# Kernel tuning notes

Measured on AMD Instinct MI355X. Metric: run time of the kernel, lower is better.

Reference implementation:

```python
import jax, jax.numpy as jnp
import numpy as np

B, C1, C2 = 8, 256, 256
Cc = 128          # c = int(c2 * e)
RED = 16          # reduction in FrequencyModulation
HEADS = 8
HD = Cc // HEADS  # 16
HH, WW = 32, 32


def _c1x1(x, w, b=None):
    # 1x1 conv as channel contraction; w: [out_c, in_c]
    y = jnp.einsum('bchw,oc->bohw', x, w)
    return y if b is None else y + b[None, :, None, None]


def setup_inputs() -> dict:
    key = jax.random.key(0)
    ks = jax.random.split(key, 22)
    s = 0.02
    p = {}
    p['x'] = jax.random.normal(ks[0], (B, C1, HH, WW), jnp.float32)
    p['cv1_w'] = jax.random.normal(ks[1], (2 * Cc, C1), jnp.float32) * s
    p['cv1_b'] = jnp.zeros((2 * Cc,), jnp.float32)
    # FrequencyModulation params
    p['fm_w1'] = jax.random.normal(ks[2], (Cc // RED, Cc), jnp.float32) * s
    p['fm_w2'] = jax.random.normal(ks[3], (Cc, Cc // RED), jnp.float32) * s
    p['ca_w1'] = jax.random.normal(ks[4], (Cc // RED, Cc), jnp.float32) * s
    p['ca_w2'] = jax.random.normal(ks[5], (Cc, Cc // RED), jnp.float32) * s
    # TokenStatisticsSelfAttention params (qkv_bias=False)
    p['qkv_w'] = jax.random.normal(ks[6], (3 * Cc, Cc), jnp.float32) * s
    p['tproj_w'] = jax.random.normal(ks[7], (Cc, Cc), jnp.float32) * s
    p['tproj_b'] = jnp.zeros((Cc,), jnp.float32)
    # SpatialQuantizedRouter params
    p['dw_w'] = jax.random.normal(ks[8], (Cc, 1, 3, 3), jnp.float32) * s  # depthwise
    p['dw_b'] = jnp.zeros((Cc,), jnp.float32)
    p['rt_w'] = jax.random.normal(ks[9], (1, Cc), jnp.float32) * s
    p['rt_b'] = jnp.zeros((1,), jnp.float32)
    p['q_w'] = jax.random.normal(ks[10], (Cc, Cc), jnp.float32) * s
    p['k_w'] = jax.random.normal(ks[11], (Cc, Cc), jnp.float32) * s
    p['v_w'] = jax.random.normal(ks[12], (Cc, Cc), jnp.float32) * s
    p['sproj_w'] = jax.random.normal(ks[13], (Cc, Cc), jnp.float32) * s
    p['sproj_b'] = jnp.zeros((Cc,), jnp.float32)
    p['cv2_w'] = jax.random.normal(ks[14], (C2, 3 * Cc), jnp.float32) * s
    p['cv2_b'] = jnp.zeros((C2,), jnp.float32)
    return p


def _forward(x, cv1_w, cv1_b, fm_w1, fm_w2, ca_w1, ca_w2, qkv_w, tproj_w,
             tproj_b, dw_w, dw_b, rt_w, rt_b, q_w, k_w, v_w, sproj_w,
             sproj_b, cv2_w, cv2_b):
    Bb, _, H, W = x.shape
    N = H * W
    y = _c1x1(x, cv1_w, cv1_b)
    y0, y1 = y[:, :Cc], y[:, Cc:]

    # ---- Branch 1: FrequencyModulation ----
    xf = jnp.fft.rfft2(y1.astype(jnp.float32), norm='ortho')  # [B,c,H,W//2+1] complex
    mag = jnp.abs(xf)
    pooled = mag.mean(axis=(-2, -1))                          # [B,c]
    fw = jax.nn.sigmoid(jax.nn.relu(pooled @ fm_w1.T) @ fm_w2.T)  # [B,c]
    # mag*fw*exp(i*phase) == fw * xf  (fw is real, per batch/channel)
    xs = jnp.fft.irfft2(xf * fw[:, :, None, None].astype(jnp.complex64),
                        s=(H, W), norm='ortho')               # [B,c,H,W]
    ca = jax.nn.sigmoid(jax.nn.relu(xs.mean(axis=(-2, -1)) @ ca_w1.T) @ ca_w2.T)
    freq_out = xs * ca[:, :, None, None]

    # ---- Branch 2: TokenStatisticsSelfAttention ----
    xt = y1.reshape(Bb, Cc, N).transpose(0, 2, 1)             # [B,N,c]
    qkv = (xt @ qkv_w.T).reshape(Bb, N, 3, HEADS, HD).transpose(2, 0, 3, 1, 4)
    q, k, v = qkv[0], qkv[1], qkv[2]                          # [B,h,N,d]
    var_v = jnp.var(v, axis=-1, ddof=1, keepdims=True)        # [B,h,N,1] (unbiased)
    var_k = jnp.var(k, axis=-1, ddof=1, keepdims=True)
    attn = jax.nn.softmax(jnp.einsum('bhnx,bhmx->bhnm', var_v, var_k) * (HD ** -0.5), axis=-1)
    to = jnp.einsum('bhnm,bhmd->bhnd', attn, v).transpose(0, 2, 1, 3).reshape(Bb, N, Cc)
    stat_out = ((to @ tproj_w.T) + tproj_b).transpose(0, 2, 1).reshape(Bb, Cc, H, W)

    # ---- Branch 3: SpatialQuantizedRouter (training-mode blend) ----
    x_local = jax.lax.conv_general_dilated(
        y1, dw_w, (1, 1), 'SAME', feature_group_count=Cc,
        dimension_numbers=('NCHW', 'OIHW', 'NCHW')) + dw_b[None, :, None, None]
    p_route = jax.nn.sigmoid(y1.mean(axis=(-2, -1)) @ rt_w.T + rt_b)  # [B,1]
    qb = jnp.sign(_c1x1(y1, q_w).reshape(Bb, Cc, N))
    kb = jnp.sign(_c1x1(y1, k_w).reshape(Bb, Cc, N))
    vv = _c1x1(y1, v_w).reshape(Bb, Cc, N)
    a2 = jax.nn.softmax(jnp.einsum('bcn,bcm->bnm', qb, kb) * (Cc ** -0.5), axis=-1)
    # torch: bmm(v, attn.T) -> out[b,c,n] = sum_m v[b,c,m]*attn[b,n,m]
    ob = jnp.einsum('bcm,bnm->bcn', vv, a2).reshape(Bb, Cc, H, W)
    out_bin = _c1x1(ob, sproj_w, sproj_b)
    alpha = p_route.reshape(Bb, 1, 1, 1)
    spat_out = (1.0 - alpha) * x_local + alpha * out_bin

    attn_out = freq_out + stat_out + spat_out
    yc = jnp.concatenate([y0, y1, attn_out], axis=1)          # [B,3c,H,W]
    out = _c1x1(yc, cv2_w, cv2_b)
    return x + out  # add: shortcut and c1 == c2


def reference(x, cv1_w, cv1_b, fm_w1, fm_w2, ca_w1, ca_w2, qkv_w, tproj_w,
              tproj_b, dw_w, dw_b, rt_w, rt_b, q_w, k_w, v_w, sproj_w,
              sproj_b, cv2_w, cv2_b):
    return _forward(x, cv1_w, cv1_b, fm_w1, fm_w2, ca_w1, ca_w2, qkv_w,
                    tproj_w, tproj_b, dw_w, dw_b, rt_w, rt_b, q_w, k_w, v_w,
                    sproj_w, sproj_b, cv2_w, cv2_b)
```

## Files before the change

kernel.cpp:

```cpp
#include <hip/hip_runtime.h>
#include <math.h>

#define BATCH 8
#define NPIX 1024

typedef __attribute__((ext_vector_type(8))) short short8v;
typedef __attribute__((ext_vector_type(4))) float f32x4;

__device__ inline unsigned short f2bf(float x) {
  unsigned int u = __float_as_uint(x);
  return (unsigned short)((u + 0x7FFFu + ((u >> 16) & 1u)) >> 16);
}
__device__ inline float bf2f(unsigned short h) {
  return __uint_as_float((unsigned int)h << 16);
}

__global__ __launch_bounds__(256) void convw_kernel(
    const float* __restrict__ cv1_w, const float* __restrict__ qkv_w,
    const float* __restrict__ tproj_w, const float* __restrict__ sproj_w,
    const float* __restrict__ cv2_w, const float* __restrict__ q_w,
    const float* __restrict__ k_w, const float* __restrict__ v_w,
    short* __restrict__ wb) {
  int i = blockIdx.x * 256 + threadIdx.x;
  float v;
  if (i < 65536) v = cv1_w[i];
  else if (i < 114688) v = qkv_w[i - 65536];
  else if (i < 131072) v = tproj_w[i - 114688];
  else if (i < 147456) v = sproj_w[i - 131072];
  else if (i < 245760) v = cv2_w[i - 147456];
  else {
    int j = i - 245760, wsel = j >> 14, r = j & 16383;
    v = (wsel == 0) ? q_w[r] : (wsel == 1) ? k_w[r] : v_w[r];
  }
  wb[i] = (short)f2bf(v);
}

__global__ __launch_bounds__(256) void tconv_kernel(
    const float* __restrict__ src, long sSrc, int C, short* __restrict__ dst) {
  __shared__ float t[64][65];
  const int b = blockIdx.z;
  const int c0 = blockIdx.x * 64, n0 = blockIdx.y * 64;
  const float* s = src + (long)b * sSrc;
  short* d = dst + (long)b * 1024 * C;
  const int tid = threadIdx.x;
#pragma unroll
  for (int p = 0; p < 16; p++) {
    int idx = tid + p * 256;
    int cl = idx >> 6, nl = idx & 63;
    t[cl][nl] = s[(long)(c0 + cl) * 1024 + n0 + nl];
  }
  __syncthreads();
#pragma unroll
  for (int p = 0; p < 16; p++) {
    int idx = tid + p * 256;
    int nl = idx >> 6, cl = idx & 63;
    d[(long)(n0 + nl) * C + c0 + cl] = (short)f2bf(t[cl][nl]);
  }
}

template<bool HAS_BIAS, bool HAS_RES, bool BF16OUT>
__global__ __launch_bounds__(256) void mgemm_kernel(
    const short* __restrict__ Wb, const short* __restrict__ XT,
    const float* __restrict__ bias, const float* __restrict__ res,
    void* __restrict__ Yv, int K, long sXT, long sY, long sR) {
  __shared__ __align__(16) short As[64][40];
  __shared__ __align__(16) short Bs[64][40];
  const int b = blockIdx.z;
  const int n0 = blockIdx.x * 64, m0 = blockIdx.y * 64;
  const int tid = threadIdx.x;
  const int l = tid & 63, w = tid >> 6;
  const int wm = w >> 1, wn = w & 1;
  const short* Xb = XT + (long)b * sXT;
  const int sr = tid >> 2, sko = (tid & 3) * 8;
  const int fr = l & 15, fk = (l >> 4) * 8;
  f32x4 acc[2][2] = {};
  for (int k0 = 0; k0 < K; k0 += 32) {
    *(uint4*)&As[sr][sko] = *(const uint4*)(Wb + (long)(m0 + sr) * K + k0 + sko);
    *(uint4*)&Bs[sr][sko] = *(const uint4*)(Xb + (long)(n0 + sr) * K + k0 + sko);
    __syncthreads();
    short8v a0 = *(short8v*)&As[wm * 32 + fr][fk];
    short8v a1 = *(short8v*)&As[wm * 32 + 16 + fr][fk];
    short8v b0 = *(short8v*)&Bs[wn * 32 + fr][fk];
    short8v b1 = *(short8v*)&Bs[wn * 32 + 16 + fr][fk];
    acc[0][0] = __builtin_amdgcn_mfma_f32_16x16x32_bf16(a0, b0, acc[0][0], 0, 0, 0);
    acc[0][1] = __builtin_amdgcn_mfma_f32_16x16x32_bf16(a0, b1, acc[0][1], 0, 0, 0);
    acc[1][0] = __builtin_amdgcn_mfma_f32_16x16x32_bf16(a1, b0, acc[1][0], 0, 0, 0);
    acc[1][1] = __builtin_amdgcn_mfma_f32_16x16x32_bf16(a1, b1, acc[1][1], 0, 0, 0);
    __syncthreads();
  }
#pragma unroll
  for (int tm = 0; tm < 2; tm++) {
#pragma unroll
    for (int i = 0; i < 4; i++) {
      int m = m0 + wm * 32 + tm * 16 + (l >> 4) * 4 + i;
      float bv = HAS_BIAS ? bias[m] : 0.f;
#pragma unroll
      for (int tn = 0; tn < 2; tn++) {
        int n = n0 + wn * 32 + tn * 16 + (l & 15);
        float v = acc[tm][tn][i] + bv;
        if (HAS_RES) v += res[(long)b * sR + (long)m * 1024 + n];
        if (BF16OUT)
          ((short*)Yv)[(long)b * sY + (long)m * 1024 + n] = (short)f2bf(v);
        else
          ((float*)Yv)[(long)b * sY + (long)m * 1024 + n] = v;
      }
    }
  }
}

__global__ __launch_bounds__(256) void fftpool_kernel(
    const float* __restrict__ yc, float* __restrict__ pooled, float* __restrict__ m1) {
  const int bc = blockIdx.x;
  const int b = bc >> 7, cx = bc & 127;
  const float* img = yc + ((long)b * 384 + 128 + cx) * NPIX;
  __shared__ float im[1024];
  __shared__ float Gr[32][17], Gi[32][17];
  __shared__ float cs[32], sn[32];
  __shared__ float red[256];
  const int t = threadIdx.x;
  if (t < 32) {
    float ang = -0.19634954084936207f * (float)t;
    __sincosf(ang, &sn[t], &cs[t]);
  }
  float lsum = 0.f;
  for (int i = t; i < 1024; i += 256) { float v = img[i]; im[i] = v; lsum += v; }
  red[t] = lsum;
  __syncthreads();
  for (int s = 128; s > 0; s >>= 1) {
    if (t < s) red[t] += red[t + s];
    __syncthreads();
  }
  if (t == 0) m1[bc] = red[0] * (1.f / 1024.f);
  for (int i = t; i < 544; i += 256) {
    int h = i / 17, v = i % 17;
    float ar = 0.f, ai = 0.f;
    for (int w2 = 0; w2 < 32; w2++) {
      int k = (v * w2) & 31;
      float x = im[h * 32 + w2];
      ar += x * cs[k]; ai += x * sn[k];
    }
    Gr[h][v] = ar; Gi[h][v] = ai;
  }
  __syncthreads();
  float asum = 0.f;
  for (int i = t; i < 544; i += 256) {
    int u = i / 17, v = i % 17;
    float xr = 0.f, xi = 0.f;
    for (int h = 0; h < 32; h++) {
      int k = (u * h) & 31;
      float gr = Gr[h][v], gi = Gi[h][v];
      xr += gr * cs[k] - gi * sn[k];
      xi += gr * sn[k] + gi * cs[k];
    }
    asum += sqrtf(xr * xr + xi * xi);
  }
  red[t] = asum;
  __syncthreads();
  for (int s = 128; s > 0; s >>= 1) {
    if (t < s) red[t] += red[t + s];
    __syncthreads();
  }
  if (t == 0) pooled[bc] = red[0] * (1.f / (32.f * 544.f));
}

__global__ __launch_bounds__(128) void gates_kernel(
    const float* __restrict__ pooled, const float* __restrict__ m1,
    const float* __restrict__ fm_w1, const float* __restrict__ fm_w2,
    const float* __restrict__ ca_w1, const float* __restrict__ ca_w2,
    const float* __restrict__ rt_w, const float* __restrict__ rt_b,
    float* __restrict__ g, float* __restrict__ alpha) {
  const int b = blockIdx.x, t = threadIdx.x;
  __shared__ float h1[8], fwv[128], xsm[128], h2[8];
  const float* pb = pooled + b * 128;
  const float* mb = m1 + b * 128;
  if (t < 8) {
    float s = 0.f;
    for (int c = 0; c < 128; c++) s += pb[c] * fm_w1[t * 128 + c];
    h1[t] = fmaxf(s, 0.f);
  }
  __syncthreads();
  {
    float s = 0.f;
    for (int r = 0; r < 8; r++) s += h1[r] * fm_w2[t * 8 + r];
    float fw = 1.f / (1.f + __expf(-s));
    fwv[t] = fw; xsm[t] = fw * mb[t];
  }
  __syncthreads();
  if (t < 8) {
    float s = 0.f;
    for (int c = 0; c < 128; c++) s += xsm[c] * ca_w1[t * 128 + c];
    h2[t] = fmaxf(s, 0.f);
  }
  __syncthreads();
  {
    float s = 0.f;
    for (int r = 0; r < 8; r++) s += h2[r] * ca_w2[t * 8 + r];
    float ca = 1.f / (1.f + __expf(-s));
    g[b * 128 + t] = fwv[t] * ca;
  }
  if (t == 0) {
    float s = 0.f;
    for (int c = 0; c < 128; c++) s += mb[c] * rt_w[c];
    s += rt_b[0];
    alpha[b] = 1.f / (1.f + __expf(-s));
  }
}

__global__ __launch_bounds__(256) void varmax_kernel(
    const float* __restrict__ qkvb, float* __restrict__ var_k,
    float* __restrict__ var_v, float* __restrict__ maxvk,
    short* __restrict__ vTb) {
  const int bh = blockIdx.x;
  const int b = bh >> 3, h = bh & 7;
  __shared__ float red[256];
  __shared__ float trans[16][256];
  const float* kb = qkvb + ((long)b * 384 + 128 + h * 16) * NPIX;
  const float* vb = qkvb + ((long)b * 384 + 256 + h * 16) * NPIX;
  float mx = 0.f;
  for (int j = 0; j < 4; j++) {
    int n = threadIdx.x + j * 256;
    float xk[16], xv[16], sk = 0.f, sv = 0.f;
#pragma unroll
    for (int d = 0; d < 16; d++) {
      xk[d] = kb[(long)d * NPIX + n]; sk += xk[d];
      xv[d] = vb[(long)d * NPIX + n]; sv += xv[d];
    }
    float mk = sk * (1.f / 16.f), mv = sv * (1.f / 16.f);
    float vk_ = 0.f, vv_ = 0.f;
#pragma unroll
    for (int d = 0; d < 16; d++) {
      float a = xk[d] - mk; vk_ += a * a;
      float c = xv[d] - mv; vv_ += c * c;
    }
    vk_ *= (1.f / 15.f); vv_ *= (1.f / 15.f);
    var_k[(long)bh * NPIX + n] = vk_;
    var_v[(long)bh * NPIX + n] = vv_;
    mx = fmaxf(mx, vk_);
#pragma unroll
    for (int d = 0; d < 16; d++) trans[d][threadIdx.x] = xv[d];
    __syncthreads();
    {
      int d = threadIdx.x >> 4, mc = threadIdx.x & 15;
      __align__(16) short tmp[16];
#pragma unroll
      for (int e = 0; e < 16; e++) tmp[e] = (short)f2bf(trans[d][mc * 16 + e]);
      short* dst = vTb + ((long)bh * 16 + d) * 1024 + j * 256 + mc * 16;
      *(uint4*)dst = *(uint4*)tmp;
      *(uint4*)(dst + 8) = *(uint4*)(tmp + 8);
    }
    __syncthreads();
  }
  red[threadIdx.x] = mx;
  __syncthreads();
  for (int s = 128; s > 0; s >>= 1) {
    if (threadIdx.x < s) red[threadIdx.x] = fmaxf(red[threadIdx.x], red[threadIdx.x + s]);
    __syncthreads();
  }
  if (threadIdx.x == 0) maxvk[bh] = red[0];
}

__global__ __launch_bounds__(256) void stat_mfma_kernel(
    const short* __restrict__ vTb, const float* __restrict__ var_k,
    const float* __restrict__ var_v, const float* __restrict__ maxvk,
    short* __restrict__ tcT) {
  const int bh = blockIdx.x;
  const int b = bh >> 3, h = bh & 7;
  const int n0 = blockIdx.y * 64;
  const int tid = threadIdx.x;
  const int l = tid & 63, w = tid >> 6;
  const int ln = l & 15, lk = l >> 4;
  const int n = n0 + w * 16 + ln;
  __shared__ float vk[1024];
  for (int i = tid; i < 1024; i += 256) vk[i] = var_k[(long)bh * 1024 + i];
  const float cn = var_v[(long)bh * 1024 + n] * 0.25f;
  const float mv = maxvk[bh];
  const short* arow = vTb + ((long)bh * 16 + ln) * 1024 + lk * 8;
  __syncthreads();
  f32x4 acc = {};
  float psum = 0.f;
  for (int m0 = 0; m0 < 1024; m0 += 32) {
    short8v afrag = *(const short8v*)(arow + m0);
    short8v bfrag;
#pragma unroll
    for (int j = 0; j < 8; j++) {
      float wv = __expf(cn * (vk[m0 + lk * 8 + j] - mv));
      psum += wv;
      bfrag[j] = (short)f2bf(wv);
    }
    acc = __builtin_amdgcn_mfma_f32_16x16x32_bf16(afrag, bfrag, acc, 0, 0, 0);
  }
  psum += __shfl_xor(psum, 16);
  psum += __shfl_xor(psum, 32);
  const float inv = 1.f / psum;
  unsigned long long pk =
      (unsigned long long)(unsigned short)f2bf(acc[0] * inv) |
      ((unsigned long long)(unsigned short)f2bf(acc[1] * inv) << 16) |
      ((unsigned long long)(unsigned short)f2bf(acc[2] * inv) << 32) |
      ((unsigned long long)(unsigned short)f2bf(acc[3] * inv) << 48);
  *(unsigned long long*)(tcT + ((long)b * 1024 + n) * 128 + h * 16 + lk * 4) = pk;
}

__global__ __launch_bounds__(256) void pack_kernel(
    const float* __restrict__ sqkv,
    unsigned long long* __restrict__ qbits, unsigned long long* __restrict__ kbits) {
  const int wave = threadIdx.x >> 6, lane = threadIdx.x & 63;
  const long p = (long)blockIdx.x * 4 + wave;
  const int b = (int)(p >> 10), n = (int)(p & 1023);
  const float* base = sqkv + (long)b * 384 * NPIX + n;
  unsigned long long q0 = __ballot(base[(long)lane * NPIX] > 0.f);
  unsigned long long q1 = __ballot(base[(long)(64 + lane) * NPIX] > 0.f);
  unsigned long long k0 = __ballot(base[(long)(128 + lane) * NPIX] > 0.f);
  unsigned long long k1 = __ballot(base[(long)(192 + lane) * NPIX] > 0.f);
  if (lane == 0) {
    qbits[p * 2] = q0; qbits[p * 2 + 1] = q1;
    kbits[p * 2] = k0; kbits[p * 2 + 1] = k1;
  }
}

__global__ __launch_bounds__(256) void obgemm_kernel(
    const short* __restrict__ pvb, const unsigned long long* __restrict__ qbits,
    const unsigned long long* __restrict__ kbits, float* __restrict__ pnum,
    float* __restrict__ pden) {
  const int b = blockIdx.z;
  const int sp = blockIdx.y;
  const int n0 = blockIdx.x * 64;
  const int kb0 = sp * 256;
  __shared__ __align__(16) short As[128][40];
  __shared__ __align__(16) unsigned long long kbsh[256][2];
  const int tid = threadIdx.x;
  const int l = tid & 63, w = tid >> 6;
  const int ln = l & 15, lk = l >> 4;
  const int n = n0 + w * 16 + ln;
  const unsigned long long q0 = qbits[((long)b * 1024 + n) * 2];
  const unsigned long long q1 = qbits[((long)b * 1024 + n) * 2 + 1];
  *(uint4*)&kbsh[tid][0] = *(const uint4*)(kbits + ((long)b * 1024 + kb0 + tid) * 2);
  const float fs = 0.08838834764831845f;
  const int sc = tid >> 1, sh = (tid & 1) * 16;
  const short* pvrow = pvb + ((long)b * 128 + sc) * 1024 + kb0;
  f32x4 acc[8] = {};
  float psum = 0.f;
  for (int ks = 0; ks < 8; ks++) {
    *(uint4*)&As[sc][sh] = *(const uint4*)(pvrow + ks * 32 + sh);
    *(uint4*)&As[sc][sh + 8] = *(const uint4*)(pvrow + ks * 32 + sh + 8);
    __syncthreads();
    const int mloc = ks * 32 + lk * 8;
    short8v bfrag;
#pragma unroll
    for (int j = 0; j < 8; j++) {
      unsigned long long kw0 = kbsh[mloc + j][0];
      unsigned long long kw1 = kbsh[mloc + j][1];
      int ham = __popcll(kw0 ^ q0) + __popcll(kw1 ^ q1);
      float wv = __expf((float)(128 - 2 * ham) * fs);
      psum += wv;
      bfrag[j] = (short)f2bf(wv);
    }
#pragma unroll
    for (int ct = 0; ct < 8; ct++) {
      short8v afrag = *(short8v*)&As[ct * 16 + ln][lk * 8];
      acc[ct] = __builtin_amdgcn_mfma_f32_16x16x32_bf16(afrag, bfrag, acc[ct], 0, 0, 0);
    }
    __syncthreads();
  }
  float* dst = pnum + (((long)sp * 8 + b) * 128) * 1024 + n;
#pragma unroll
  for (int ct = 0; ct < 8; ct++)
#pragma unroll
    for (int i = 0; i < 4; i++)
      dst[(long)(ct * 16 + lk * 4 + i) * 1024] = acc[ct][i];
  psum += __shfl_xor(psum, 16);
  psum += __shfl_xor(psum, 32);
  if (lk == 0)
    pden[((long)sp * 8 + b) * 1024 + n] = psum;
}

__global__ __launch_bounds__(256) void dwcombine_kernel(
    float* __restrict__ yc, const float* __restrict__ dw_w,
    const float* __restrict__ dw_b, const float* __restrict__ pnum,
    const float* __restrict__ pden, const float* __restrict__ sproj_b,
    const float* __restrict__ g, const float* __restrict__ alpha) {
  const int bc = blockIdx.x;
  const int b = bc >> 7, cx = bc & 127;
  const float* img = yc + ((long)b * 384 + 128 + cx) * NPIX;
  float* dst = yc + ((long)b * 384 + 256 + cx) * NPIX;
  float w[9];
#pragma unroll
  for (int i = 0; i < 9; i++) w[i] = dw_w[cx * 9 + i];
  const float bias = dw_b[cx];
  const float a = alpha[b];
  const float gg = g[bc];
  const float sb = sproj_b[cx];
  const long ns = 8L * 128 * 1024;
  const long ds = 8L * 1024;
  const long nbase = ((long)b * 128 + cx) * 1024;
  const long dbase = (long)b * 1024;
  for (int i = threadIdx.x; i < 1024; i += 256) {
    int h = i >> 5, wx = i & 31;
    float s = bias;
#pragma unroll
    for (int ky = 0; ky < 3; ky++) {
      int hh = h + ky - 1;
      if (hh < 0 || hh > 31) continue;
#pragma unroll
      for (int kx = 0; kx < 3; kx++) {
        int ww2 = wx + kx - 1;
        if (ww2 < 0 || ww2 > 31) continue;
        s += img[hh * 32 + ww2] * w[ky * 3 + kx];
      }
    }
    float num = pnum[nbase + i] + pnum[nbase + i + ns] +
                pnum[nbase + i + 2 * ns] + pnum[nbase + i + 3 * ns];
    float den = pden[dbase + i] + pden[dbase + i + ds] +
                pden[dbase + i + 2 * ds] + pden[dbase + i + 3 * ds];
    float obv = num / den + sb;
    dst[i] = dst[i] + gg * img[i] + (1.f - a) * s + a * obv;
  }
}

extern "C" void kernel_launch(void* const* d_in, const int* in_sizes, int n_in,
                              void* d_out, int out_size, void* d_ws, size_t ws_size,
                              hipStream_t stream) {
  const float* x = (const float*)d_in[0];
  const float* cv1_w = (const float*)d_in[1];
  const float* cv1_b = (const float*)d_in[2];
  const float* fm_w1 = (const float*)d_in[3];
  const float* fm_w2 = (const float*)d_in[4];
  const float* ca_w1 = (const float*)d_in[5];
  const float* ca_w2 = (const float*)d_in[6];
  const float* qkv_w = (const float*)d_in[7];
  const float* tproj_w = (const float*)d_in[8];
  const float* tproj_b = (const float*)d_in[9];
  const float* dw_w = (const float*)d_in[10];
  const float* dw_b = (const float*)d_in[11];
  const float* rt_w = (const float*)d_in[12];
  const float* rt_b = (const float*)d_in[13];
  const float* q_w = (const float*)d_in[14];
  const float* k_w = (const float*)d_in[15];
  const float* v_w = (const float*)d_in[16];
  const float* sproj_w = (const float*)d_in[17];
  const float* sproj_b = (const float*)d_in[18];
  const float* cv2_w = (const float*)d_in[19];
  const float* cv2_b = (const float*)d_in[20];
  float* out = (float*)d_out;

  char* wsp = (char*)d_ws;
  size_t off = 0;
  auto alloc = [&](size_t bytes) {
    void* p = wsp + off;
    off += (bytes + 255) & ~(size_t)255;
    return p;
  };
  float* yc = (float*)alloc(8UL * 384 * 1024 * 4);
  float* qkvb = (float*)alloc(8UL * 384 * 1024 * 4);
  float* pn_t = (float*)alloc(8UL * 128 * 1024 * 4);
  float* sqkv = (float*)alloc(8UL * 384 * 1024 * 4);
  float* pv = (float*)alloc(8UL * 128 * 1024 * 4);
  short* xT = (short*)alloc(8UL * 1024 * 256 * 2);
  short* y1T = (short*)alloc(8UL * 1024 * 128 * 2);
  short* tcT = (short*)alloc(8UL * 1024 * 128 * 2);
  short* vvT = (short*)alloc(8UL * 1024 * 128 * 2);
  short* wb = (short*)alloc(294912UL * 2);
  short* vTb = (short*)alloc(64UL * 16 * 1024 * 2);
  float* pden = (float*)alloc(4UL * 8 * 1024 * 4);
  float* var_k = (float*)alloc(8UL * 8 * 1024 * 4);
  float* var_v = (float*)alloc(8UL * 8 * 1024 * 4);
  float* maxvk = (float*)alloc(64 * 4);
  float* pooled = (float*)alloc(1024 * 4);
  float* m1 = (float*)alloc(1024 * 4);
  float* g = (float*)alloc(1024 * 4);
  float* alpha = (float*)alloc(8 * 4);
  unsigned long long* qbits = (unsigned long long*)alloc(8192UL * 2 * 8);
  unsigned long long* kbits = (unsigned long long*)alloc(8192UL * 2 * 8);
  (void)pn_t;
  float* pnum = qkvb;
  short* pvb = (short*)pv;
  short* ycT = xT;
  const short* cv1b = wb;
  const short* qkvwb = wb + 65536;
  const short* tprojb = wb + 114688;
  const short* sprojb = wb + 131072;
  const short* cv2b = wb + 147456;
  const short* skvb = wb + 245760;
  if (off > ws_size) return;

  dim3 blk(256);
  convw_kernel<<<dim3(1152), blk, 0, stream>>>(cv1_w, qkv_w, tproj_w, sproj_w,
                                               cv2_w, q_w, k_w, v_w, wb);
  tconv_kernel<<<dim3(4, 16, 8), blk, 0, stream>>>(x, 256L * 1024, 256, xT);
  mgemm_kernel<true, false, false><<<dim3(16, 4, 8), blk, 0, stream>>>(
      cv1b, xT, cv1_b, nullptr, yc, 256, 1024L * 256, 384L * 1024, 0);
  fftpool_kernel<<<dim3(1024), blk, 0, stream>>>(yc, pooled, m1);
  gates_kernel<<<dim3(8), dim3(128), 0, stream>>>(pooled, m1, fm_w1, fm_w2,
                                                  ca_w1, ca_w2, rt_w, rt_b, g, alpha);
  tconv_kernel<<<dim3(2, 16, 8), blk, 0, stream>>>(yc + 128 * 1024, 384L * 1024,
                                                   128, y1T);
  mgemm_kernel<false, false, false><<<dim3(16, 6, 8), blk, 0, stream>>>(
      qkvwb, y1T, nullptr, nullptr, qkvb, 128, 1024L * 128, 384L * 1024, 0);
  varmax_kernel<<<dim3(64), blk, 0, stream>>>(qkvb, var_k, var_v, maxvk, vTb);
  stat_mfma_kernel<<<dim3(64, 16), blk, 0, stream>>>(vTb, var_k, var_v, maxvk, tcT);
  mgemm_kernel<true, false, false><<<dim3(16, 2, 8), blk, 0, stream>>>(
      tprojb, tcT, tproj_b, nullptr, yc + 256 * 1024, 128, 1024L * 128,
      384L * 1024, 0);
  mgemm_kernel<false, false, false><<<dim3(16, 6, 8), blk, 0, stream>>>(
      skvb, y1T, nullptr, nullptr, sqkv, 128, 1024L * 128, 384L * 1024, 0);
  pack_kernel<<<dim3(2048), blk, 0, stream>>>(sqkv, qbits, kbits);
  tconv_kernel<<<dim3(2, 16, 8), blk, 0, stream>>>(sqkv + 256 * 1024,
                                                   384L * 1024, 128, vvT);
  mgemm_kernel<false, false, true><<<dim3(16, 2, 8), blk, 0, stream>>>(
      sprojb, vvT, nullptr, nullptr, pvb, 128, 1024L * 128, 128L * 1024, 0);
  obgemm_kernel<<<dim3(16, 4, 8), blk, 0, stream>>>(pvb, qbits, kbits, pnum, pden);
  dwcombine_kernel<<<dim3(1024), blk, 0, stream>>>(yc, dw_w, dw_b, pnum, pden,
                                                   sproj_b, g, alpha);
  tconv_kernel<<<dim3(6, 16, 8), blk, 0, stream>>>(yc, 384L * 1024, 384, ycT);
  mgemm_kernel<true, true, false><<<dim3(16, 4, 8), blk, 0, stream>>>(
      cv2b, ycT, cv2_b, x, out, 384, 1024L * 384, 256L * 1024, 256L * 1024);
}
```

Measured before the change: 149.1 us.

## Emit transposed bf16 outputs from GEMM epilogues and merge qkv/spatial GEMMs

The cv1 GEMM now writes bf16 transposed (pixel-major) y0/y1 straight into the final concat buffer, plus an fp32 y1 copy. This removes two transpose-convert kernels. The qkv and spatial q/k/v projections are merged into one GEMM launch with 768 output rows: the first 384 go to fp32 for the statistics branch and the rest go to transposed bf16 for the binary branch, which pack_kernel and the sproj GEMM then read directly. Only the attention output still needs a transpose, at the cost of scattered 8-byte epilogue stores and sign bits now derived from bf16-rounded values.

Result: faster. 125.9 us (-15.6%).

```diff
diff --git a/kernel.cpp b/kernel.cpp
--- a/kernel.cpp
+++ b/kernel.cpp
@@ -13,6 +13,12 @@
 }
 __device__ inline float bf2f(unsigned short h) {
   return __uint_as_float((unsigned int)h << 16);
+}
+__device__ inline unsigned long long pack4bf(float a, float b, float c, float d) {
+  return (unsigned long long)(unsigned short)f2bf(a) |
+         ((unsigned long long)(unsigned short)f2bf(b) << 16) |
+         ((unsigned long long)(unsigned short)f2bf(c) << 32) |
+         ((unsigned long long)(unsigned short)f2bf(d) << 48);
 }
 
 __global__ __launch_bounds__(256) void convw_kernel(
@@ -24,24 +30,28 @@
   int i = blockIdx.x * 256 + threadIdx.x;
   float v;
   if (i < 65536) v = cv1_w[i];
-  else if (i < 114688) v = qkv_w[i - 65536];
-  else if (i < 131072) v = tproj_w[i - 114688];
-  else if (i < 147456) v = sproj_w[i - 131072];
-  else if (i < 245760) v = cv2_w[i - 147456];
-  else {
-    int j = i - 245760, wsel = j >> 14, r = j & 16383;
-    v = (wsel == 0) ? q_w[r] : (wsel == 1) ? k_w[r] : v_w[r];
-  }
+  else if (i < 163840) {
+    int j = i - 65536;
+    if (j < 49152) v = qkv_w[j];
+    else {
+      int jj = j - 49152, wsel = jj >> 14, r = jj & 16383;
+      v = (wsel == 0) ? q_w[r] : (wsel == 1) ? k_w[r] : v_w[r];
+    }
+  }
+  else if (i < 180224) v = tproj_w[i - 163840];
+  else if (i < 196608) v = sproj_w[i - 180224];
+  else v = cv2_w[i - 196608];
   wb[i] = (short)f2bf(v);
 }
 
 __global__ __launch_bounds__(256) void tconv_kernel(
-    const float* __restrict__ src, long sSrc, int C, short* __restrict__ dst) {
+    const float* __restrict__ src, long sSrc, int dstStride, int dstOff,
+    short* __restrict__ dst) {
   __shared__ float t[64][65];
   const int b = blockIdx.z;
   const int c0 = blockIdx.x * 64, n0 = blockIdx.y * 64;
   const float* s = src + (long)b * sSrc;
-  short* d = dst + (long)b * 1024 * C;
+  short* d = dst + (long)b * 1024 * dstStride;
   const int tid = threadIdx.x;
 #pragma unroll
   for (int p = 0; p < 16; p++) {
@@ -54,15 +64,16 @@
   for (int p = 0; p < 16; p++) {
     int idx = tid + p * 256;
     int nl = idx >> 6, cl = idx & 63;
-    d[(long)(n0 + nl) * C + c0 + cl] = (short)f2bf(t[cl][nl]);
-  }
-}
-
-template<bool HAS_BIAS, bool HAS_RES, bool BF16OUT>
+    d[(long)(n0 + nl) * dstStride + dstOff + c0 + cl] = (short)f2bf(t[cl][nl]);
+  }
+}
+
+template<int MODE, bool HAS_BIAS, bool HAS_RES>
 __global__ __launch_bounds__(256) void mgemm_kernel(
-    const short* __restrict__ Wb, const short* __restrict__ XT,
+    const short* __restrict__ Wb, const short* __restrict__ XT, int ldx,
     const float* __restrict__ bias, const float* __restrict__ res,
-    void* __restrict__ Yv, int K, long sXT, long sY, long sR) {
+    void* __restrict__ Y0, void* __restrict__ Y1,
+    int K, long sXT, long sY, long sR) {
   __shared__ __align__(16) short As[64][40];
   __shared__ __align__(16) short Bs[64][40];
   const int b = blockIdx.z;
@@ -76,7 +87,7 @@
   f32x4 acc[2][2] = {};
   for (int k0 = 0; k0 < K; k0 += 32) {
     *(uint4*)&As[sr][sko] = *(const uint4*)(Wb + (long)(m0 + sr) * K + k0 + sko);
-    *(uint4*)&Bs[sr][sko] = *(const uint4*)(Xb + (long)(n0 + sr) * K + k0 + sko);
+    *(uint4*)&Bs[sr][sko] = *(const uint4*)(Xb + (long)(n0 + sr) * ldx + k0 + sko);
     __syncthreads();
     short8v a0 = *(short8v*)&As[wm * 32 + fr][fk];
     short8v a1 = *(short8v*)&As[wm * 32 + 16 + fr][fk];
@@ -90,29 +101,58 @@
   }
 #pragma unroll
   for (int tm = 0; tm < 2; tm++) {
-#pragma unroll
-    for (int i = 0; i < 4; i++) {
-      int m = m0 + wm * 32 + tm * 16 + (l >> 4) * 4 + i;
-      float bv = HAS_BIAS ? bias[m] : 0.f;
-#pragma unroll
-      for (int tn = 0; tn < 2; tn++) {
-        int n = n0 + wn * 32 + tn * 16 + (l & 15);
-        float v = acc[tm][tn][i] + bv;
-        if (HAS_RES) v += res[(long)b * sR + (long)m * 1024 + n];
-        if (BF16OUT)
-          ((short*)Yv)[(long)b * sY + (long)m * 1024 + n] = (short)f2bf(v);
-        else
-          ((float*)Yv)[(long)b * sY + (long)m * 1024 + n] = v;
+    const int m_base = m0 + wm * 32 + tm * 16 + (l >> 4) * 4;
+#pragma unroll
+    for (int tn = 0; tn < 2; tn++) {
+      const int n = n0 + wn * 32 + tn * 16 + (l & 15);
+      float v0 = acc[tm][tn][0], v1 = acc[tm][tn][1];
+      float v2 = acc[tm][tn][2], v3 = acc[tm][tn][3];
+      if (HAS_BIAS) {
+        v0 += bias[m_base]; v1 += bias[m_base + 1];
+        v2 += bias[m_base + 2]; v3 += bias[m_base + 3];
       }
+      if (MODE == 0 || MODE == 1) {
+        if (HAS_RES) {
+          v0 += res[(long)b * sR + (long)(m_base + 0) * 1024 + n];
+          v1 += res[(long)b * sR + (long)(m_base + 1) * 1024 + n];
+          v2 += res[(long)b * sR + (long)(m_base + 2) * 1024 + n];
+          v3 += res[(long)b * sR + (long)(m_base + 3) * 1024 + n];
+        }
+        if (MODE == 0) {
+          float* Y = (float*)Y0 + (long)b * sY + n;
+          Y[(long)(m_base + 0) * 1024] = v0; Y[(long)(m_base + 1) * 1024] = v1;
+          Y[(long)(m_base + 2) * 1024] = v2; Y[(long)(m_base + 3) * 1024] = v3;
+        } else {
+          short* Y = (short*)Y0 + (long)b * sY + n;
+          Y[(long)(m_base + 0) * 1024] = (short)f2bf(v0);
+          Y[(long)(m_base + 1) * 1024] = (short)f2bf(v1);
+          Y[(long)(m_base + 2) * 1024] = (short)f2bf(v2);
+          Y[(long)(m_base + 3) * 1024] = (short)f2bf(v3);
+        }
+      } else if (MODE == 2) {
+        *(unsigned long long*)((short*)Y0 + ((long)b * 1024 + n) * 384 + m_base) =
+            pack4bf(v0, v1, v2, v3);
+        if (m_base >= 128) {
+          float* Y = (float*)Y1 + ((long)b * 128 + m_base - 128) * 1024 + n;
+          Y[0] = v0; Y[1024] = v1; Y[2048] = v2; Y[3072] = v3;
+        }
+      } else {
+        if (m0 < 384) {
+          float* Y = (float*)Y0 + (long)b * 384 * 1024 + (long)m_base * 1024 + n;
+          Y[0] = v0; Y[1024] = v1; Y[2048] = v2; Y[3072] = v3;
+        } else {
+          *(unsigned long long*)((short*)Y1 + ((long)b * 1024 + n) * 384 +
+                                 (m_base - 384)) = pack4bf(v0, v1, v2, v3);
+        }
+      }
     }
   }
 }
 
 __global__ __launch_bounds__(256) void fftpool_kernel(
-    const float* __restrict__ yc, float* __restrict__ pooled, float* __restrict__ m1) {
+    const float* __restrict__ y1, float* __restrict__ pooled, float* __restrict__ m1) {
   const int bc = blockIdx.x;
-  const int b = bc >> 7, cx = bc & 127;
-  const float* img = yc + ((long)b * 384 + 128 + cx) * NPIX;
+  const float* img = y1 + (long)bc * NPIX;
   __shared__ float im[1024];
   __shared__ float Gr[32][17], Gi[32][17];
   __shared__ float cs[32], sn[32];
@@ -292,25 +332,20 @@
   psum += __shfl_xor(psum, 16);
   psum += __shfl_xor(psum, 32);
   const float inv = 1.f / psum;
-  unsigned long long pk =
-      (unsigned long long)(unsigned short)f2bf(acc[0] * inv) |
-      ((unsigned long long)(unsigned short)f2bf(acc[1] * inv) << 16) |
-      ((unsigned long long)(unsigned short)f2bf(acc[2] * inv) << 32) |
-      ((unsigned long long)(unsigned short)f2bf(acc[3] * inv) << 48);
-  *(unsigned long long*)(tcT + ((long)b * 1024 + n) * 128 + h * 16 + lk * 4) = pk;
+  *(unsigned long long*)(tcT + ((long)b * 1024 + n) * 128 + h * 16 + lk * 4) =
+      pack4bf(acc[0] * inv, acc[1] * inv, acc[2] * inv, acc[3] * inv);
 }
 
 __global__ __launch_bounds__(256) void pack_kernel(
-    const float* __restrict__ sqkv,
+    const short* __restrict__ sqkvT,
     unsigned long long* __restrict__ qbits, unsigned long long* __restrict__ kbits) {
   const int wave = threadIdx.x >> 6, lane = threadIdx.x & 63;
   const long p = (long)blockIdx.x * 4 + wave;
-  const int b = (int)(p >> 10), n = (int)(p & 1023);
-  const float* base = sqkv + (long)b * 384 * NPIX + n;
-  unsigned long long q0 = __ballot(base[(long)lane * NPIX] > 0.f);
-  unsigned long long q1 = __ballot(base[(long)(64 + lane) * NPIX] > 0.f);
-  unsigned long long k0 = __ballot(base[(long)(128 + lane) * NPIX] > 0.f);
-  unsigned long long k1 = __ballot(base[(long)(192 + lane) * NPIX] > 0.f);
+  const short* base = sqkvT + p * 384;
+  unsigned long long q0 = __ballot(bf2f((unsigned short)base[lane]) > 0.f);
+  unsigned long long q1 = __ballot(bf2f((unsigned short)base[64 + lane]) > 0.f);
+  unsigned long long k0 = __ballot(bf2f((unsigned short)base[128 + lane]) > 0.f);
+  unsigned long long k1 = __ballot(bf2f((unsigned short)base[192 + lane]) > 0.f);
   if (lane == 0) {
     qbits[p * 2] = q0; qbits[p * 2 + 1] = q1;
     kbits[p * 2] = k0; kbits[p * 2 + 1] = k1;
@@ -374,14 +409,15 @@
 }
 
 __global__ __launch_bounds__(256) void dwcombine_kernel(
-    float* __restrict__ yc, const float* __restrict__ dw_w,
-    const float* __restrict__ dw_b, const float* __restrict__ pnum,
-    const float* __restrict__ pden, const float* __restrict__ sproj_b,
-    const float* __restrict__ g, const float* __restrict__ alpha) {
+    const float* __restrict__ y1, float* __restrict__ attn,
+    const float* __restrict__ dw_w, const float* __restrict__ dw_b,
+    const float* __restrict__ pnum, const float* __restrict__ pden,
+    const float* __restrict__ sproj_b, const float* __restrict__ g,
+    const float* __restrict__ alpha) {
   const int bc = blockIdx.x;
   const int b = bc >> 7, cx = bc & 127;
-  const float* img = yc + ((long)b * 384 + 128 + cx) * NPIX;
-  float* dst = yc + ((long)b * 384 + 256 + cx) * NPIX;
+  const float* img = y1 + (long)bc * NPIX;
+  float* dst = attn + (long)bc * NPIX;
   float w[9];
 #pragma unroll
   for (int i = 0; i < 9; i++) w[i] = dw_w[cx * 9 + i];
@@ -391,7 +427,7 @@
   const float sb = sproj_b[cx];
   const long ns = 8L * 128 * 1024;
   const long ds = 8L * 1024;
-  const long nbase = ((long)b * 128 + cx) * 1024;
+  const long nbase = (long)bc * 1024;
   const long dbase = (long)b * 1024;
   for (int i = threadIdx.x; i < 1024; i += 256) {
     int h = i >> 5, wx = i & 31;
@@ -449,15 +485,15 @@
     off += (bytes + 255) & ~(size_t)255;
     return p;
   };
-  float* yc = (float*)alloc(8UL * 384 * 1024 * 4);
   float* qkvb = (float*)alloc(8UL * 384 * 1024 * 4);
   float* pn_t = (float*)alloc(8UL * 128 * 1024 * 4);
-  float* sqkv = (float*)alloc(8UL * 384 * 1024 * 4);
-  float* pv = (float*)alloc(8UL * 128 * 1024 * 4);
+  float* y1 = (float*)alloc(8UL * 128 * 1024 * 4);
+  float* attn = (float*)alloc(8UL * 128 * 1024 * 4);
+  short* ycT = (short*)alloc(8UL * 1024 * 384 * 2);
+  short* sqkvT = (short*)alloc(8UL * 1024 * 384 * 2);
   short* xT = (short*)alloc(8UL * 1024 * 256 * 2);
-  short* y1T = (short*)alloc(8UL * 1024 * 128 * 2);
   short* tcT = (short*)alloc(8UL * 1024 * 128 * 2);
-  short* vvT = (short*)alloc(8UL * 1024 * 128 * 2);
+  short* pvb = (short*)alloc(8UL * 128 * 1024 * 2);
   short* wb = (short*)alloc(294912UL * 2);
   short* vTb = (short*)alloc(64UL * 16 * 1024 * 2);
   float* pden = (float*)alloc(4UL * 8 * 1024 * 4);
@@ -472,45 +508,38 @@
   unsigned long long* kbits = (unsigned long long*)alloc(8192UL * 2 * 8);
   (void)pn_t;
   float* pnum = qkvb;
-  short* pvb = (short*)pv;
-  short* ycT = xT;
   const short* cv1b = wb;
-  const short* qkvwb = wb + 65536;
-  const short* tprojb = wb + 114688;
-  const short* sprojb = wb + 131072;
-  const short* cv2b = wb + 147456;
-  const short* skvb = wb + 245760;
+  const short* qsb = wb + 65536;
+  const short* tprojb = wb + 163840;
+  const short* sprojb = wb + 180224;
+  const short* cv2b = wb + 196608;
   if (off > ws_size) return;
 
   dim3 blk(256);
   convw_kernel<<<dim3(1152), blk, 0, stream>>>(cv1_w, qkv_w, tproj_w, sproj_w,
                                                cv2_w, q_w, k_w, v_w, wb);
-  tconv_kernel<<<dim3(4, 16, 8), blk, 0, stream>>>(x, 256L * 1024, 256, xT);
-  mgemm_kernel<true, false, false><<<dim3(16, 4, 8), blk, 0, stream>>>(
-      cv1b, xT, cv1_b, nullptr, yc, 256, 1024L * 256, 384L * 1024, 0);
-  fftpool_kernel<<<dim3(1024), blk, 0, stream>>>(yc, pooled, m1);
+  tconv_kernel<<<dim3(4, 16, 8), blk, 0, stream>>>(x, 256L * 1024, 256, 0, xT);
+  mgemm_kernel<2, true, false><<<dim3(16, 4, 8), blk, 0, stream>>>(
+      cv1b, xT, 256, cv1_b, nullptr, ycT, y1, 256, 1024L * 256, 0, 0);
+  fftpool_kernel<<<dim3(1024), blk, 0, stream>>>(y1, pooled, m1);
   gates_kernel<<<dim3(8), dim3(128), 0, stream>>>(pooled, m1, fm_w1, fm_w2,
                                                   ca_w1, ca_w2, rt_w, rt_b, g, alpha);
-  tconv_kernel<<<dim3(2, 16, 8), blk, 0, stream>>>(yc + 128 * 1024, 384L * 1024,
-                                                   128, y1T);
-  mgemm_kernel<false, false, false><<<dim3(16, 6, 8), blk, 0, stream>>>(
-      qkvwb, y1T, nullptr, nullptr, qkvb, 128, 1024L * 128, 384L * 1024, 0);
+  mgemm_kernel<3, false, false><<<dim3(16, 12, 8), blk, 0, stream>>>(
+      qsb, ycT + 128, 384, nullptr, nullptr, qkvb, sqkvT, 128, 1024L * 384, 0, 0);
   varmax_kernel<<<dim3(64), blk, 0, stream>>>(qkvb, var_k, var_v, maxvk, vTb);
   stat_mfma_kernel<<<dim3(64, 16), blk, 0, stream>>>(vTb, var_k, var_v, maxvk, tcT);
-  mgemm_kernel<true, false, false><<<dim3(16, 2, 8), blk, 0, stream>>>(
-      tprojb, tcT, tproj_b, nullptr, yc + 256 * 1024, 128, 1024L * 128,
-      384L * 1024, 0);
-  mgemm_kernel<false, false, false><<<dim3(16, 6, 8), blk, 0, stream>>>(
-      skvb, y1T, nullptr, nullptr, sqkv, 128, 1024L * 128, 384L * 1024, 0);
-  pack_kernel<<<dim3(2048), blk, 0, stream>>>(sqkv, qbits, kbits);
-  tconv_kernel<<<dim3(2, 16, 8), blk, 0, stream>>>(sqkv + 256 * 1024,
-                                                   384L * 1024, 128, vvT);
-  mgemm_kernel<false, false, true><<<dim3(16, 2, 8), blk, 0, stream>>>(
-      sprojb, vvT, nullptr, nullptr, pvb, 128, 1024L * 128, 128L * 1024, 0);
+  mgemm_kernel<0, true, false><<<dim3(16, 2, 8), blk, 0, stream>>>(
+      tprojb, tcT, 128, tproj_b, nullptr, attn, nullptr, 128, 1024L * 128,
+      128L * 1024, 0);
+  pack_kernel<<<dim3(2048), blk, 0, stream>>>(sqkvT, qbits, kbits);
+  mgemm_kernel<1, false, false><<<dim3(16, 2, 8), blk, 0, stream>>>(
+      sprojb, sqkvT + 256, 384, nullptr, nullptr, pvb, nullptr, 128,
+      1024L * 384, 128L * 1024, 0);
   obgemm_kernel<<<dim3(16, 4, 8), blk, 0, stream>>>(pvb, qbits, kbits, pnum, pden);
-  dwcombine_kernel<<<dim3(1024), blk, 0, stream>>>(yc, dw_w, dw_b, pnum, pden,
-                                                   sproj_b, g, alpha);
-  tconv_kernel<<<dim3(6, 16, 8), blk, 0, stream>>>(yc, 384L * 1024, 384, ycT);
-  mgemm_kernel<true, true, false><<<dim3(16, 4, 8), blk, 0, stream>>>(
-      cv2b, ycT, cv2_b, x, out, 384, 1024L * 384, 256L * 1024, 256L * 1024);
-}
+  dwcombine_kernel<<<dim3(1024), blk, 0, stream>>>(y1, attn, dw_w, dw_b, pnum,
+                                                   pden, sproj_b, g, alpha);
+  tconv_kernel<<<dim3(2, 16, 8), blk, 0, stream>>>(attn, 128L * 1024, 384, 256, ycT);
+  mgemm_kernel<0, true, true><<<dim3(16, 4, 8), blk, 0, stream>>>(
+      cv2b, ycT, 384, cv2_b, x, out, nullptr, 384, 1024L * 384, 256L * 1024,
+      256L * 1024);
+}
```
